# Kernel optimization log

Hardware: AMD Instinct MI355X
Metric: run time of the kernel (lower is better)

Reference implementation:

```python
import jax, jax.numpy as jnp
import numpy as np

H = 1024      # hidden_size
I = 2048      # intermediate_size
E = 8         # num_local_experts
TOP_K = 2     # num_experts_per_tok
B, S = 2, 2048


def setup_inputs() -> dict:
    key = jax.random.key(0)
    ks = jax.random.split(key, 9)
    sc = 0.02
    return {
        "hidden_states": jax.random.normal(ks[0], (B, S, H), dtype=jnp.float32),
        "router_w": jax.random.normal(ks[1], (H, E), dtype=jnp.float32) * sc,
        "gate_w": jax.random.normal(ks[2], (E, H, I), dtype=jnp.float32) * sc,
        "up_w": jax.random.normal(ks[3], (E, H, I), dtype=jnp.float32) * sc,
        "down_w": jax.random.normal(ks[4], (E, I, H), dtype=jnp.float32) * sc,
        "shared_gate_w": jax.random.normal(ks[5], (H, I), dtype=jnp.float32) * sc,
        "shared_up_w": jax.random.normal(ks[6], (H, I), dtype=jnp.float32) * sc,
        "shared_down_w": jax.random.normal(ks[7], (I, H), dtype=jnp.float32) * sc,
    }


def reference(hidden_states, router_w, gate_w, up_w, down_w,
              shared_gate_w, shared_up_w, shared_down_w):
    b, s, h = hidden_states.shape
    T = b * s
    x = hidden_states.reshape(T, h)

    # Router
    router_logits = x @ router_w                                   # [T, E]
    router_probs = jax.nn.softmax(router_logits.astype(jnp.float32), axis=-1).astype(x.dtype)
    topk_w, topk_i = jax.lax.top_k(router_probs, TOP_K)            # [T, K]
    topk_w = topk_w / jnp.sum(topk_w, axis=-1, keepdims=True)

    # Combine weights: combine[t, e] = sum of normalized top-k weight routed to expert e
    rows = jnp.arange(T)[:, None]
    combine = jnp.zeros((T, E), dtype=x.dtype).at[rows, topk_i].add(topk_w)  # [T, E]

    # Dense per-expert SwiGLU (combine weight is 0 for non-selected tokens, so
    # this matches the original gather-MLP-scatter math exactly)
    gate = jax.nn.silu(jnp.einsum('th,ehi->tei', x, gate_w))       # [T, E, I]
    up = jnp.einsum('th,ehi->tei', x, up_w)                        # [T, E, I]
    expert_out = jnp.einsum('tei,eih->teh', gate * up, down_w)     # [T, E, H]
    routed = jnp.einsum('te,teh->th', combine, expert_out)         # [T, H]

    # Shared expert (num_shared_experts = 1, mean over 1 is identity)
    shared = (jax.nn.silu(x @ shared_gate_w) * (x @ shared_up_w)) @ shared_down_w
    routed = routed + shared

    # Load-balance aux loss
    dispatch = jax.nn.one_hot(topk_i, E, dtype=jnp.float32).sum(axis=1) / float(TOP_K)  # [T, E]
    tokens_per_expert = dispatch.mean(axis=0)
    prob_per_expert = router_probs.astype(jnp.float32).mean(axis=0)
    aux_loss = E * jnp.sum(tokens_per_expert * prob_per_expert)

    # Router z-loss
    z_loss = jnp.mean(jax.nn.logsumexp(router_logits.astype(jnp.float32), axis=-1) ** 2)

    return (routed.reshape(b, s, h), aux_loss, z_loss,
            router_logits.reshape(b, s, E))
```

## Files before the change

### kernel.cpp

```cpp
#include <hip/hip_runtime.h>
#include <hip/hip_bf16.h>
#include <stdint.h>
#include <stddef.h>

typedef __bf16 bf16;
typedef __bf16 bf16x8 __attribute__((ext_vector_type(8)));
typedef __bf16 bf16x4 __attribute__((ext_vector_type(4)));
typedef float f32x4 __attribute__((ext_vector_type(4)));

#define HID 1024
#define IDIM 2048
#define NE 8
#define NTOK 4096
#define NSLOT 12800
#define SH_BASE 8704
#define MAX_TILES 200

#define WS_META    0
#define WS_PERM    4096
#define WS_TOKE    55296
#define WS_TOKW    88064
#define WS_SLOTOF  120832
#define WS_GATET   153600
#define WS_UPT     33708032
#define WS_DOWNT   67262464
#define WS_SGT     100816896
#define WS_SUT     105011200
#define WS_SDT     109205504
#define WS_ACT     113399808
#define WS_DOUT    165828608

#define M_CNT 0
#define M_CUR 8
#define M_PSUM 16
#define M_ZSUM 24
#define M_AOFF 32
#define M_NTILE 48
#define M_TE 64
#define M_TB 320

#define OUT_AUX 4194304
#define OUT_Z   4194305
#define OUT_LG  4194306

__device__ __forceinline__ int imin(int a, int b) { return a < b ? a : b; }

typedef const __attribute__((address_space(1))) uint32_t* as1_u32p;
typedef __attribute__((address_space(3))) uint32_t* as3_u32p;

__device__ __forceinline__ void gload16(const void* g, void* l) {
    __builtin_amdgcn_global_load_lds((as1_u32p)g, (as3_u32p)l, 16, 0, 0);
}

__global__ void zero_kernel(uint32_t* meta) {
    if (threadIdx.x < 32) meta[threadIdx.x] = 0;
}

__global__ __launch_bounds__(1024) void router_kernel(
    const float* __restrict__ x, const float* __restrict__ rw,
    float* __restrict__ out, uint32_t* meta, int* tok_e, float* tok_w,
    bf16* __restrict__ xbf)
{
    __shared__ float s_psum[NE];
    __shared__ float s_zsum;
    __shared__ uint32_t s_cnt[NE];
    int tid = threadIdx.x;
    if (tid < NE) { s_psum[tid] = 0.f; s_cnt[tid] = 0u; }
    if (tid == NE) s_zsum = 0.f;
    __syncthreads();

    int lane = tid & 63, wv = tid >> 6;
    int t = blockIdx.x * 16 + wv;
    float acc[NE];
#pragma unroll
    for (int e = 0; e < NE; e++) acc[e] = 0.f;
#pragma unroll
    for (int it = 0; it < 4; it++) {
        int h0 = (lane + it * 64) * 4;
        f32x4 xv = *(const f32x4*)&x[(size_t)t * HID + h0];
        bf16x4 xb;
#pragma unroll
        for (int j = 0; j < 4; j++) xb[j] = (bf16)xv[j];
        *(bf16x4*)&xbf[(size_t)t * HID + h0] = xb;
#pragma unroll
        for (int j = 0; j < 4; j++) {
            float xf = xv[j];
            const float* wrow = rw + (size_t)(h0 + j) * NE;
            f32x4 w0 = *(const f32x4*)wrow;
            f32x4 w1 = *(const f32x4*)(wrow + 4);
#pragma unroll
            for (int e = 0; e < 4; e++) { acc[e] += xf * w0[e]; acc[e + 4] += xf * w1[e]; }
        }
    }
#pragma unroll
    for (int off = 32; off >= 1; off >>= 1)
#pragma unroll
        for (int e = 0; e < NE; e++) acc[e] += __shfl_xor(acc[e], off);

    if (lane == 0) {
        float mx = acc[0];
        for (int e = 1; e < NE; e++) mx = fmaxf(mx, acc[e]);
        float p[NE], s = 0.f;
        for (int e = 0; e < NE; e++) { p[e] = __expf(acc[e] - mx); s += p[e]; }
        float lse = mx + __logf(s);
        atomicAdd(&s_zsum, lse * lse);
        float inv = 1.f / s;
        for (int e = 0; e < NE; e++) {
            p[e] *= inv;
            atomicAdd(&s_psum[e], p[e]);
            out[(size_t)OUT_LG + (size_t)t * NE + e] = acc[e];
        }
        int e0 = 0;
        for (int e = 1; e < NE; e++) if (p[e] > p[e0]) e0 = e;
        int e1 = (e0 == 0) ? 1 : 0;
        for (int e = 0; e < NE; e++) if (e != e0 && p[e] > p[e1]) e1 = e;
        float wn = 1.f / (p[e0] + p[e1]);
        tok_e[2 * t] = e0; tok_e[2 * t + 1] = e1;
        tok_w[2 * t] = p[e0] * wn; tok_w[2 * t + 1] = p[e1] * wn;
        atomicAdd(&s_cnt[e0], 1u);
        atomicAdd(&s_cnt[e1], 1u);
    }
    __syncthreads();
    if (tid < NE) {
        atomicAdd((float*)&meta[M_PSUM + tid], s_psum[tid]);
        atomicAdd(&meta[M_CNT + tid], s_cnt[tid]);
    }
    if (tid == NE) atomicAdd((float*)&meta[M_ZSUM], s_zsum);
}

__global__ void offsets_kernel(uint32_t* meta, float* out) {
    if (threadIdx.x != 0 || blockIdx.x != 0) return;
    uint32_t off = 0, idx = 0;
    for (int e = 0; e < NE; e++) {
        meta[M_AOFF + e] = off;
        uint32_t c = meta[M_CNT + e];
        uint32_t nt = (c + 63) >> 6;
        for (uint32_t j = 0; j < nt && idx < MAX_TILES; j++) {
            meta[M_TE + idx] = e;
            meta[M_TB + idx] = off + j * 64;
            idx++;
        }
        off += nt * 64;
    }
    meta[M_AOFF + NE] = off;
    for (uint32_t j = 0; j < NTOK / 64 && idx < MAX_TILES; j++) {
        meta[M_TE + idx] = NE;
        meta[M_TB + idx] = SH_BASE + j * 64;
        idx++;
    }
    meta[M_NTILE] = idx;
    float aux = 0.f;
    for (int e = 0; e < NE; e++) {
        float tpe = (float)meta[M_CNT + e] / (2.f * NTOK);
        float ppe = ((float*)meta)[M_PSUM + e] / (float)NTOK;
        aux += tpe * ppe;
    }
    out[OUT_AUX] = aux * NE;
    out[OUT_Z] = ((float*)meta)[M_ZSUM] / (float)NTOK;
}

__global__ void fill_kernel(uint32_t* perm) {
    int g = blockIdx.x * 256 + threadIdx.x;
    if (g < NSLOT) perm[g] = (g < SH_BASE) ? 0u : (uint32_t)(g - SH_BASE);
}

__global__ void dispatch_kernel(uint32_t* meta, const int* tok_e,
                                uint32_t* perm, uint32_t* slot_of) {
    int t = blockIdx.x * 256 + threadIdx.x;
    int lane = threadIdx.x & 63;
    for (int k = 0; k < 2; k++) {
        int e = tok_e[2 * t + k] & 7;
#pragma unroll
        for (int ee = 0; ee < NE; ee++) {
            bool mine = (e == ee);
            unsigned long long mask = __ballot(mine);
            if (mask == 0ull) continue;
            int leader = __ffsll((unsigned long long)mask) - 1;
            uint32_t wbase = 0;
            if (lane == leader)
                wbase = atomicAdd(&meta[M_CUR + ee], (uint32_t)__popcll(mask));
            wbase = __shfl(wbase, leader);
            if (mine) {
                uint32_t myrank = (uint32_t)__popcll(mask & ((1ull << lane) - 1ull));
                uint32_t slot = meta[M_AOFF + ee] + wbase + myrank;
                if (slot >= NSLOT) slot = 0;
                perm[slot] = (uint32_t)t;
                slot_of[2 * t + k] = slot;
            }
        }
    }
}

__device__ __forceinline__ size_t f_off(int n, int k, int KB32) {
    return ((size_t)((n >> 5) * KB32 + (k >> 5)) * 2 + ((n >> 4) & 1)) * 512
         + (size_t)((((k >> 3) & 3) * 16 + (n & 15)) * 8);
}

__global__ __launch_bounds__(256) void transpose_kernel(
    const float* gw, const float* uw, const float* dw,
    const float* sg, const float* su, const float* sd, char* ws)
{
    int mat = blockIdx.x >> 9, tile = blockIdx.x & 511;
    const float* src; bf16* dst; int R, C;
    const size_t MSZ = (size_t)HID * IDIM;
    if (mat < 8)       { src = gw + mat * MSZ;        dst = (bf16*)(ws + WS_GATET) + mat * MSZ; R = HID;  C = IDIM; }
    else if (mat < 16) { src = uw + (mat - 8) * MSZ;  dst = (bf16*)(ws + WS_UPT) + (mat - 8) * MSZ; R = HID; C = IDIM; }
    else if (mat < 24) { src = dw + (mat - 16) * MSZ; dst = (bf16*)(ws + WS_DOWNT) + (mat - 16) * MSZ; R = IDIM; C = HID; }
    else if (mat == 24){ src = sg; dst = (bf16*)(ws + WS_SGT); R = HID; C = IDIM; }
    else if (mat == 25){ src = su; dst = (bf16*)(ws + WS_SUT); R = HID; C = IDIM; }
    else               { src = sd; dst = (bf16*)(ws + WS_SDT); R = IDIM; C = HID; }
    int KB32 = R >> 5;
    int tpr = C >> 6;
    int r0 = (tile / tpr) * 64, c0 = (tile % tpr) * 64;
    __shared__ bf16 tl[64][65];
    int tid = threadIdx.x;
#pragma unroll
    for (int it = 0; it < 4; it++) {
        int idx = tid + it * 256;
        int r = idx >> 4, c4 = (idx & 15) * 4;
        f32x4 v = *(const f32x4*)&src[(size_t)(r0 + r) * C + c0 + c4];
#pragma unroll
        for (int j = 0; j < 4; j++) tl[c4 + j][r] = (bf16)v[j];
    }
    __syncthreads();
#pragma unroll
    for (int it = 0; it < 2; it++) {
        int idx = tid + it * 256;
        int rr = idx >> 3, c8 = (idx & 7) * 8;
        int n = c0 + rr, k = r0 + c8;
        bf16x8 o;
#pragma unroll
        for (int j = 0; j < 8; j++) o[j] = tl[rr][c8 + j];
        *(bf16x8*)&dst[f_off(n, k, KB32)] = o;
    }
}

__global__ __launch_bounds__(256) void stage1_kernel(char* __restrict__ ws)
{
    uint32_t* meta = (uint32_t*)(ws + WS_META);
    int mtile = blockIdx.y;
    int ntile = imin((int)meta[M_NTILE], MAX_TILES);
    if (mtile >= ntile) return;
    int e = imin((int)meta[M_TE + mtile], NE);
    int slot0 = imin((int)meta[M_TB + mtile], NSLOT - 64);
    if (slot0 < 0) slot0 = 0;
    const bf16* BgF = (e < NE) ? (const bf16*)(ws + WS_GATET) + (size_t)e * HID * IDIM
                               : (const bf16*)(ws + WS_SGT);
    const bf16* BuF = (e < NE) ? (const bf16*)(ws + WS_UPT) + (size_t)e * HID * IDIM
                               : (const bf16*)(ws + WS_SUT);
    const uint32_t* perm = (const uint32_t*)(ws + WS_PERM);
    const bf16* xbf = (const bf16*)(ws + WS_DOUT);
    bf16* act = (bf16*)(ws + WS_ACT);

    __shared__ bf16 As[4096];
    __shared__ bf16 Bgs[8192];
    __shared__ bf16 Bus[8192];

    int tid = threadIdx.x, lane = tid & 63, wv = tid >> 6;
    int q = lane >> 4, m = lane & 15;

    int tok = (int)(perm[slot0 + wv * 16 + m] & (NTOK - 1));
    const bf16* gA = xbf + (size_t)tok * HID + q * 8;
    int N32 = blockIdx.x * 4 + wv;
    const bf16* gBg = BgF + (size_t)N32 * 32768 + lane * 8;
    const bf16* gBu = BuF + (size_t)N32 * 32768 + lane * 8;

    f32x4 zero4 = {0.f, 0.f, 0.f, 0.f};
    f32x4 accg[4][2], accu[4][2];
#pragma unroll
    for (int a = 0; a < 4; a++)
#pragma unroll
        for (int b = 0; b < 2; b++) { accg[a][b] = zero4; accu[a][b] = zero4; }

    for (int k0 = 0; k0 < HID; k0 += 64) {
        int kc = k0 >> 5;
        gload16(gA + k0,      &As[(wv * 2 + 0) * 512]);
        gload16(gA + k0 + 32, &As[(wv * 2 + 1) * 512]);
#pragma unroll
        for (int nt = 0; nt < 2; nt++)
#pragma unroll
            for (int kk = 0; kk < 2; kk++) {
                size_t so = (size_t)(kc + kk) * 1024 + nt * 512;
                gload16(gBg + so, &Bgs[((wv * 2 + nt) * 2 + kk) * 512]);
                gload16(gBu + so, &Bus[((wv * 2 + nt) * 2 + kk) * 512]);
            }
        __syncthreads();
#pragma unroll
        for (int kk = 0; kk < 2; kk++) {
            bf16x8 af[4];
#pragma unroll
            for (int m4 = 0; m4 < 4; m4++)
                af[m4] = *(bf16x8*)&As[((m4 * 2 + kk) * 64 + lane) * 8];
#pragma unroll
            for (int nt = 0; nt < 2; nt++) {
                bf16x8 bg = *(bf16x8*)&Bgs[(((wv * 2 + nt) * 2 + kk) * 64 + lane) * 8];
                bf16x8 bu = *(bf16x8*)&Bus[(((wv * 2 + nt) * 2 + kk) * 64 + lane) * 8];
#pragma unroll
                for (int m4 = 0; m4 < 4; m4++) {
                    accg[m4][nt] = __builtin_amdgcn_mfma_f32_16x16x32_bf16(af[m4], bg, accg[m4][nt], 0, 0, 0);
                    accu[m4][nt] = __builtin_amdgcn_mfma_f32_16x16x32_bf16(af[m4], bu, accu[m4][nt], 0, 0, 0);
                }
            }
        }
        __syncthreads();
    }
    size_t tb = (size_t)(slot0 >> 6) * 64;
#pragma unroll
    for (int m4 = 0; m4 < 4; m4++)
#pragma unroll
        for (int nt = 0; nt < 2; nt++) {
            int col = blockIdx.x * 128 + wv * 32 + nt * 16 + m;
            size_t base = ((tb + (col >> 5)) * 4 + m4) * 512
                        + (size_t)((((col >> 3) & 3) * 16) * 8) + (col & 7);
#pragma unroll
            for (int r = 0; r < 4; r++) {
                float g = accg[m4][nt][r], u = accu[m4][nt][r];
                float v = g / (1.f + __expf(-g)) * u;
                act[base + (size_t)(q * 4 + r) * 8] = (bf16)v;
            }
        }
}

__global__ __launch_bounds__(256) void stage2_kernel(char* __restrict__ ws)
{
    uint32_t* meta = (uint32_t*)(ws + WS_META);
    int mtile = blockIdx.y;
    int ntile = imin((int)meta[M_NTILE], MAX_TILES);
    if (mtile >= ntile) return;
    int e = imin((int)meta[M_TE + mtile], NE);
    int slot0 = imin((int)meta[M_TB + mtile], NSLOT - 64);
    if (slot0 < 0) slot0 = 0;
    int n0 = blockIdx.x * 128;
    const bf16* BF = (e < NE) ? (const bf16*)(ws + WS_DOWNT) + (size_t)e * HID * IDIM
                              : (const bf16*)(ws + WS_SDT);
    const bf16* actF = (const bf16*)(ws + WS_ACT);
    bf16* dout = (bf16*)(ws + WS_DOUT);

    __shared__ bf16 As[4096];
    __shared__ bf16 Bs[8192];

    int tid = threadIdx.x, lane = tid & 63, wv = tid >> 6;
    int q = lane >> 4, m = lane & 15;

    int tile = slot0 >> 6;
    const bf16* gA = actF + ((size_t)tile * 64 * 4 + wv) * 512 + lane * 8;
    int N32 = blockIdx.x * 4 + wv;
    const bf16* gB = BF + (size_t)N32 * 65536 + lane * 8;

    f32x4 zero4 = {0.f, 0.f, 0.f, 0.f};
    f32x4 acc[4][2];
#pragma unroll
    for (int a = 0; a < 4; a++)
#pragma unroll
        for (int b = 0; b < 2; b++) acc[a][b] = zero4;

    for (int k0 = 0; k0 < IDIM; k0 += 64) {
        int kc = k0 >> 5;
#pragma unroll
        for (int kk = 0; kk < 2; kk++)
            gload16(gA + (size_t)(kc + kk) * 2048, &As[(wv * 2 + kk) * 512]);
#pragma unroll
        for (int nt = 0; nt < 2; nt++)
#pragma unroll
            for (int kk = 0; kk < 2; kk++)
                gload16(gB + (size_t)(kc + kk) * 1024 + nt * 512,
                        &Bs[((wv * 2 + nt) * 2 + kk) * 512]);
        __syncthreads();
#pragma unroll
        for (int kk = 0; kk < 2; kk++) {
            bf16x8 af[4];
#pragma unroll
            for (int m4 = 0; m4 < 4; m4++)
                af[m4] = *(bf16x8*)&As[((m4 * 2 + kk) * 64 + lane) * 8];
#pragma unroll
            for (int nt = 0; nt < 2; nt++) {
                bf16x8 bfr = *(bf16x8*)&Bs[(((wv * 2 + nt) * 2 + kk) * 64 + lane) * 8];
#pragma unroll
                for (int m4 = 0; m4 < 4; m4++)
                    acc[m4][nt] = __builtin_amdgcn_mfma_f32_16x16x32_bf16(af[m4], bfr, acc[m4][nt], 0, 0, 0);
            }
        }
        __syncthreads();
    }
#pragma unroll
    for (int m4 = 0; m4 < 4; m4++)
#pragma unroll
        for (int nt = 0; nt < 2; nt++)
#pragma unroll
            for (int r = 0; r < 4; r++) {
                int slot = slot0 + m4 * 16 + q * 4 + r;
                int col = n0 + wv * 32 + nt * 16 + m;
                dout[(size_t)slot * HID + col] = (bf16)acc[m4][nt][r];
            }
}

__global__ __launch_bounds__(256) void combine_kernel(char* __restrict__ ws, float* __restrict__ out)
{
    int g = blockIdx.x * 256 + threadIdx.x;
    int t = g >> 7;
    int hc = (g & 127) * 8;
    const uint32_t* slot_of = (const uint32_t*)(ws + WS_SLOTOF);
    const float* tok_w = (const float*)(ws + WS_TOKW);
    const bf16* dout = (const bf16*)(ws + WS_DOUT);
    uint32_t s0 = slot_of[2 * t], s1 = slot_of[2 * t + 1];
    if (s0 >= NSLOT) s0 = 0;
    if (s1 >= NSLOT) s1 = 0;
    float w0 = tok_w[2 * t], w1 = tok_w[2 * t + 1];
    bf16x8 a = *(const bf16x8*)&dout[(size_t)s0 * HID + hc];
    bf16x8 b = *(const bf16x8*)&dout[(size_t)s1 * HID + hc];
    bf16x8 c = *(const bf16x8*)&dout[(size_t)(SH_BASE + t) * HID + hc];
    f32x4 o0, o1;
#pragma unroll
    for (int j = 0; j < 4; j++)
        o0[j] = w0 * (float)a[j] + w1 * (float)b[j] + (float)c[j];
#pragma unroll
    for (int j = 0; j < 4; j++)
        o1[j] = w0 * (float)a[j + 4] + w1 * (float)b[j + 4] + (float)c[j + 4];
    *(f32x4*)&out[(size_t)t * HID + hc] = o0;
    *(f32x4*)&out[(size_t)t * HID + hc + 4] = o1;
}

extern "C" void kernel_launch(void* const* d_in, const int* in_sizes, int n_in,
                              void* d_out, int out_size, void* d_ws, size_t ws_size,
                              hipStream_t stream) {
    const float* x  = (const float*)d_in[0];
    const float* rw = (const float*)d_in[1];
    const float* gw = (const float*)d_in[2];
    const float* uw = (const float*)d_in[3];
    const float* dw = (const float*)d_in[4];
    const float* sg = (const float*)d_in[5];
    const float* su = (const float*)d_in[6];
    const float* sd = (const float*)d_in[7];
    float* out = (float*)d_out;
    char* ws = (char*)d_ws;
    uint32_t* meta = (uint32_t*)(ws + WS_META);
    uint32_t* perm = (uint32_t*)(ws + WS_PERM);
    int* tok_e = (int*)(ws + WS_TOKE);
    float* tok_w = (float*)(ws + WS_TOKW);
    uint32_t* slot_of = (uint32_t*)(ws + WS_SLOTOF);
    bf16* xbf = (bf16*)(ws + WS_DOUT);

    hipLaunchKernelGGL(zero_kernel, dim3(1), dim3(64), 0, stream, meta);
    hipLaunchKernelGGL(router_kernel, dim3(NTOK / 16), dim3(1024), 0, stream,
                       x, rw, out, meta, tok_e, tok_w, xbf);
    hipLaunchKernelGGL(offsets_kernel, dim3(1), dim3(64), 0, stream, meta, out);
    hipLaunchKernelGGL(fill_kernel, dim3((NSLOT + 255) / 256), dim3(256), 0, stream, perm);
    hipLaunchKernelGGL(dispatch_kernel, dim3(NTOK / 256), dim3(256), 0, stream,
                       meta, tok_e, perm, slot_of);
    hipLaunchKernelGGL(transpose_kernel, dim3(27 * 512), dim3(256), 0, stream,
                       gw, uw, dw, sg, su, sd, ws);
    hipLaunchKernelGGL(stage1_kernel, dim3(IDIM / 128, MAX_TILES), dim3(256), 0, stream, ws);
    hipLaunchKernelGGL(stage2_kernel, dim3(HID / 128, MAX_TILES), dim3(256), 0, stream, ws);
    hipLaunchKernelGGL(combine_kernel, dim3(NTOK * HID / 8 / 256), dim3(256), 0, stream, ws, out);
}
```

Measured before the change: 550.4 us.

## Double M-tile to 128 rows in expert GEMMs and re-layout workspace

Raises the per-block token tile from 64 to 128 rows in both the gate/up and down GEMM stages, so each loaded weight tile is reused across twice as many tokens and weight traffic from memory is halved. Expert slot padding and tile metadata now use 128-row granularity, and offset computation is parallelised across lanes. The bf16 copy of x gets its own buffer, and the down-projection output now shares space with the transposed gate weights. In exchange, each block needs more accumulator registers and LDS (launch bounds hint 2 and 3 blocks per CU), padding waste grows, and there are fewer blocks to fill the device.

```diff
diff --git a/kernel.cpp b/kernel.cpp
--- a/kernel.cpp
+++ b/kernel.cpp
@@ -12,23 +12,24 @@
 #define IDIM 2048
 #define NE 8
 #define NTOK 4096
-#define NSLOT 12800
-#define SH_BASE 8704
-#define MAX_TILES 200
+#define NSLOT 13312
+#define SH_BASE 9216
+#define MAX_TILES 104
 
 #define WS_META    0
 #define WS_PERM    4096
-#define WS_TOKE    55296
-#define WS_TOKW    88064
-#define WS_SLOTOF  120832
-#define WS_GATET   153600
-#define WS_UPT     33708032
-#define WS_DOWNT   67262464
-#define WS_SGT     100816896
-#define WS_SUT     105011200
-#define WS_SDT     109205504
-#define WS_ACT     113399808
-#define WS_DOUT    165828608
+#define WS_TOKE    57344
+#define WS_TOKW    90112
+#define WS_SLOTOF  122880
+#define WS_XBF     155648
+#define WS_GATET   8544256
+#define WS_UPT     42098688
+#define WS_DOWNT   75653120
+#define WS_SGT     109207552
+#define WS_SUT     113401856
+#define WS_SDT     117596160
+#define WS_ACT     121790464
+#define WS_DOUT    WS_GATET
 
 #define M_CNT 0
 #define M_CUR 8
@@ -129,34 +130,39 @@
 }
 
 __global__ void offsets_kernel(uint32_t* meta, float* out) {
-    if (threadIdx.x != 0 || blockIdx.x != 0) return;
-    uint32_t off = 0, idx = 0;
-    for (int e = 0; e < NE; e++) {
-        meta[M_AOFF + e] = off;
-        uint32_t c = meta[M_CNT + e];
-        uint32_t nt = (c + 63) >> 6;
-        for (uint32_t j = 0; j < nt && idx < MAX_TILES; j++) {
+    __shared__ uint32_t s_aoff[NE + 1];
+    int lane = threadIdx.x;
+    if (lane == 0) {
+        uint32_t off = 0;
+        for (int e = 0; e < NE; e++) {
+            meta[M_AOFF + e] = off; s_aoff[e] = off;
+            off += ((meta[M_CNT + e] + 127) >> 7) << 7;
+        }
+        meta[M_AOFF + NE] = off; s_aoff[NE] = off;
+        float aux = 0.f;
+        for (int e = 0; e < NE; e++) {
+            float tpe = (float)meta[M_CNT + e] / (2.f * NTOK);
+            float ppe = ((float*)meta)[M_PSUM + e] / (float)NTOK;
+            aux += tpe * ppe;
+        }
+        out[OUT_AUX] = aux * NE;
+        out[OUT_Z] = ((float*)meta)[M_ZSUM] / (float)NTOK;
+    }
+    __syncthreads();
+    uint32_t nrt = s_aoff[NE] >> 7;
+    uint32_t ntile = nrt + NTOK / 128;
+    if (lane == 0) meta[M_NTILE] = ntile;
+    for (uint32_t idx = lane; idx < ntile && idx < MAX_TILES; idx += 64) {
+        if (idx < nrt) {
+            uint32_t base = idx << 7, e = 0;
+            for (int j = 1; j < NE; j++) if (base >= s_aoff[j]) e = j;
             meta[M_TE + idx] = e;
-            meta[M_TB + idx] = off + j * 64;
-            idx++;
-        }
-        off += nt * 64;
-    }
-    meta[M_AOFF + NE] = off;
-    for (uint32_t j = 0; j < NTOK / 64 && idx < MAX_TILES; j++) {
-        meta[M_TE + idx] = NE;
-        meta[M_TB + idx] = SH_BASE + j * 64;
-        idx++;
-    }
-    meta[M_NTILE] = idx;
-    float aux = 0.f;
-    for (int e = 0; e < NE; e++) {
-        float tpe = (float)meta[M_CNT + e] / (2.f * NTOK);
-        float ppe = ((float*)meta)[M_PSUM + e] / (float)NTOK;
-        aux += tpe * ppe;
-    }
-    out[OUT_AUX] = aux * NE;
-    out[OUT_Z] = ((float*)meta)[M_ZSUM] / (float)NTOK;
+            meta[M_TB + idx] = base;
+        } else {
+            meta[M_TE + idx] = NE;
+            meta[M_TB + idx] = SH_BASE + ((idx - nrt) << 7);
+        }
+    }
 }
 
 __global__ void fill_kernel(uint32_t* perm) {
@@ -235,47 +241,51 @@
     }
 }
 
-__global__ __launch_bounds__(256) void stage1_kernel(char* __restrict__ ws)
+__global__ __launch_bounds__(256, 2) void stage1_kernel(char* __restrict__ ws)
 {
     uint32_t* meta = (uint32_t*)(ws + WS_META);
     int mtile = blockIdx.y;
     int ntile = imin((int)meta[M_NTILE], MAX_TILES);
     if (mtile >= ntile) return;
     int e = imin((int)meta[M_TE + mtile], NE);
-    int slot0 = imin((int)meta[M_TB + mtile], NSLOT - 64);
+    int slot0 = imin((int)meta[M_TB + mtile], NSLOT - 128);
     if (slot0 < 0) slot0 = 0;
     const bf16* BgF = (e < NE) ? (const bf16*)(ws + WS_GATET) + (size_t)e * HID * IDIM
                                : (const bf16*)(ws + WS_SGT);
     const bf16* BuF = (e < NE) ? (const bf16*)(ws + WS_UPT) + (size_t)e * HID * IDIM
                                : (const bf16*)(ws + WS_SUT);
     const uint32_t* perm = (const uint32_t*)(ws + WS_PERM);
-    const bf16* xbf = (const bf16*)(ws + WS_DOUT);
+    const bf16* xbf = (const bf16*)(ws + WS_XBF);
     bf16* act = (bf16*)(ws + WS_ACT);
 
-    __shared__ bf16 As[4096];
+    __shared__ bf16 As[8192];
     __shared__ bf16 Bgs[8192];
     __shared__ bf16 Bus[8192];
 
     int tid = threadIdx.x, lane = tid & 63, wv = tid >> 6;
     int q = lane >> 4, m = lane & 15;
 
-    int tok = (int)(perm[slot0 + wv * 16 + m] & (NTOK - 1));
-    const bf16* gA = xbf + (size_t)tok * HID + q * 8;
+    int tok0 = (int)(perm[slot0 + wv * 16 + m] & (NTOK - 1));
+    int tok1 = (int)(perm[slot0 + (wv + 4) * 16 + m] & (NTOK - 1));
+    const bf16* gA0 = xbf + (size_t)tok0 * HID + q * 8;
+    const bf16* gA1 = xbf + (size_t)tok1 * HID + q * 8;
     int N32 = blockIdx.x * 4 + wv;
     const bf16* gBg = BgF + (size_t)N32 * 32768 + lane * 8;
     const bf16* gBu = BuF + (size_t)N32 * 32768 + lane * 8;
 
     f32x4 zero4 = {0.f, 0.f, 0.f, 0.f};
-    f32x4 accg[4][2], accu[4][2];
-#pragma unroll
-    for (int a = 0; a < 4; a++)
+    f32x4 accg[8][2], accu[8][2];
+#pragma unroll
+    for (int a = 0; a < 8; a++)
 #pragma unroll
         for (int b = 0; b < 2; b++) { accg[a][b] = zero4; accu[a][b] = zero4; }
 
     for (int k0 = 0; k0 < HID; k0 += 64) {
         int kc = k0 >> 5;
-        gload16(gA + k0,      &As[(wv * 2 + 0) * 512]);
-        gload16(gA + k0 + 32, &As[(wv * 2 + 1) * 512]);
+        gload16(gA0 + k0,      &As[(wv * 2 + 0) * 512]);
+        gload16(gA0 + k0 + 32, &As[(wv * 2 + 1) * 512]);
+        gload16(gA1 + k0,      &As[((wv + 4) * 2 + 0) * 512]);
+        gload16(gA1 + k0 + 32, &As[((wv + 4) * 2 + 1) * 512]);
 #pragma unroll
         for (int nt = 0; nt < 2; nt++)
 #pragma unroll
@@ -287,48 +297,50 @@
         __syncthreads();
 #pragma unroll
         for (int kk = 0; kk < 2; kk++) {
-            bf16x8 af[4];
-#pragma unroll
-            for (int m4 = 0; m4 < 4; m4++)
-                af[m4] = *(bf16x8*)&As[((m4 * 2 + kk) * 64 + lane) * 8];
+            bf16x8 af[8];
+#pragma unroll
+            for (int mc = 0; mc < 8; mc++)
+                af[mc] = *(bf16x8*)&As[((mc * 2 + kk) * 64 + lane) * 8];
 #pragma unroll
             for (int nt = 0; nt < 2; nt++) {
                 bf16x8 bg = *(bf16x8*)&Bgs[(((wv * 2 + nt) * 2 + kk) * 64 + lane) * 8];
                 bf16x8 bu = *(bf16x8*)&Bus[(((wv * 2 + nt) * 2 + kk) * 64 + lane) * 8];
 #pragma unroll
-                for (int m4 = 0; m4 < 4; m4++) {
-                    accg[m4][nt] = __builtin_amdgcn_mfma_f32_16x16x32_bf16(af[m4], bg, accg[m4][nt], 0, 0, 0);
-                    accu[m4][nt] = __builtin_amdgcn_mfma_f32_16x16x32_bf16(af[m4], bu, accu[m4][nt], 0, 0, 0);
+                for (int mc = 0; mc < 8; mc++) {
+                    accg[mc][nt] = __builtin_amdgcn_mfma_f32_16x16x32_bf16(af[mc], bg, accg[mc][nt], 0, 0, 0);
+                    accu[mc][nt] = __builtin_amdgcn_mfma_f32_16x16x32_bf16(af[mc], bu, accu[mc][nt], 0, 0, 0);
                 }
             }
         }
         __syncthreads();
     }
-    size_t tb = (size_t)(slot0 >> 6) * 64;
-#pragma unroll
-    for (int m4 = 0; m4 < 4; m4++)
+    int tile = slot0 >> 7;
+    int kcell = blockIdx.x * 4 + wv;
+    size_t tbase = (size_t)tile * 262144;
+#pragma unroll
+    for (int mc = 0; mc < 8; mc++)
 #pragma unroll
         for (int nt = 0; nt < 2; nt++) {
-            int col = blockIdx.x * 128 + wv * 32 + nt * 16 + m;
-            size_t base = ((tb + (col >> 5)) * 4 + m4) * 512
-                        + (size_t)((((col >> 3) & 3) * 16) * 8) + (col & 7);
+            int kc2 = nt * 2 + (m >> 3);
+            size_t base = tbase + (size_t)(kcell * 8 + mc) * 512
+                        + (size_t)(kc2 * 16) * 8 + (m & 7);
 #pragma unroll
             for (int r = 0; r < 4; r++) {
-                float g = accg[m4][nt][r], u = accu[m4][nt][r];
+                float g = accg[mc][nt][r], u = accu[mc][nt][r];
                 float v = g / (1.f + __expf(-g)) * u;
                 act[base + (size_t)(q * 4 + r) * 8] = (bf16)v;
             }
         }
 }
 
-__global__ __launch_bounds__(256) void stage2_kernel(char* __restrict__ ws)
+__global__ __launch_bounds__(256, 3) void stage2_kernel(char* __restrict__ ws)
 {
     uint32_t* meta = (uint32_t*)(ws + WS_META);
     int mtile = blockIdx.y;
     int ntile = imin((int)meta[M_NTILE], MAX_TILES);
     if (mtile >= ntile) return;
     int e = imin((int)meta[M_TE + mtile], NE);
-    int slot0 = imin((int)meta[M_TB + mtile], NSLOT - 64);
+    int slot0 = imin((int)meta[M_TB + mtile], NSLOT - 128);
     if (slot0 < 0) slot0 = 0;
     int n0 = blockIdx.x * 128;
     const bf16* BF = (e < NE) ? (const bf16*)(ws + WS_DOWNT) + (size_t)e * HID * IDIM
@@ -336,29 +348,32 @@
     const bf16* actF = (const bf16*)(ws + WS_ACT);
     bf16* dout = (bf16*)(ws + WS_DOUT);
 
-    __shared__ bf16 As[4096];
+    __shared__ bf16 As[8192];
     __shared__ bf16 Bs[8192];
 
     int tid = threadIdx.x, lane = tid & 63, wv = tid >> 6;
     int q = lane >> 4, m = lane & 15;
 
-    int tile = slot0 >> 6;
-    const bf16* gA = actF + ((size_t)tile * 64 * 4 + wv) * 512 + lane * 8;
+    int tile = slot0 >> 7;
+    size_t tbase = (size_t)tile * 262144;
+    const bf16* gA = actF + tbase + lane * 8;
     int N32 = blockIdx.x * 4 + wv;
     const bf16* gB = BF + (size_t)N32 * 65536 + lane * 8;
 
     f32x4 zero4 = {0.f, 0.f, 0.f, 0.f};
-    f32x4 acc[4][2];
-#pragma unroll
-    for (int a = 0; a < 4; a++)
+    f32x4 acc[8][2];
+#pragma unroll
+    for (int a = 0; a < 8; a++)
 #pragma unroll
         for (int b = 0; b < 2; b++) acc[a][b] = zero4;
 
     for (int k0 = 0; k0 < IDIM; k0 += 64) {
         int kc = k0 >> 5;
 #pragma unroll
-        for (int kk = 0; kk < 2; kk++)
-            gload16(gA + (size_t)(kc + kk) * 2048, &As[(wv * 2 + kk) * 512]);
+        for (int kk = 0; kk < 2; kk++) {
+            gload16(gA + (size_t)((kc + kk) * 8 + wv) * 512,     &As[(wv * 2 + kk) * 512]);
+            gload16(gA + (size_t)((kc + kk) * 8 + wv + 4) * 512, &As[((wv + 4) * 2 + kk) * 512]);
+        }
 #pragma unroll
         for (int nt = 0; nt < 2; nt++)
 #pragma unroll
@@ -368,29 +383,29 @@
         __syncthreads();
 #pragma unroll
         for (int kk = 0; kk < 2; kk++) {
-            bf16x8 af[4];
-#pragma unroll
-            for (int m4 = 0; m4 < 4; m4++)
-                af[m4] = *(bf16x8*)&As[((m4 * 2 + kk) * 64 + lane) * 8];
+            bf16x8 af[8];
+#pragma unroll
+            for (int mc = 0; mc < 8; mc++)
+                af[mc] = *(bf16x8*)&As[((mc * 2 + kk) * 64 + lane) * 8];
 #pragma unroll
             for (int nt = 0; nt < 2; nt++) {
                 bf16x8 bfr = *(bf16x8*)&Bs[(((wv * 2 + nt) * 2 + kk) * 64 + lane) * 8];
 #pragma unroll
-                for (int m4 = 0; m4 < 4; m4++)
-                    acc[m4][nt] = __builtin_amdgcn_mfma_f32_16x16x32_bf16(af[m4], bfr, acc[m4][nt], 0, 0, 0);
+                for (int mc = 0; mc < 8; mc++)
+                    acc[mc][nt] = __builtin_amdgcn_mfma_f32_16x16x32_bf16(af[mc], bfr, acc[mc][nt], 0, 0, 0);
             }
         }
         __syncthreads();
     }
 #pragma unroll
-    for (int m4 = 0; m4 < 4; m4++)
+    for (int mc = 0; mc < 8; mc++)
 #pragma unroll
         for (int nt = 0; nt < 2; nt++)
 #pragma unroll
             for (int r = 0; r < 4; r++) {
-                int slot = slot0 + m4 * 16 + q * 4 + r;
+                int slot = slot0 + mc * 16 + q * 4 + r;
                 int col = n0 + wv * 32 + nt * 16 + m;
-                dout[(size_t)slot * HID + col] = (bf16)acc[m4][nt][r];
+                dout[(size_t)slot * HID + col] = (bf16)acc[mc][nt][r];
             }
 }
 
@@ -438,7 +453,7 @@
     int* tok_e = (int*)(ws + WS_TOKE);
     float* tok_w = (float*)(ws + WS_TOKW);
     uint32_t* slot_of = (uint32_t*)(ws + WS_SLOTOF);
-    bf16* xbf = (bf16*)(ws + WS_DOUT);
+    bf16* xbf = (bf16*)(ws + WS_XBF);
 
     hipLaunchKernelGGL(zero_kernel, dim3(1), dim3(64), 0, stream, meta);
     hipLaunchKernelGGL(router_kernel, dim3(NTOK / 16), dim3(1024), 0, stream,
```

Measured after the change: 509.1 us. 1.08x faster.
